# Performance work log

Hardware: AMD Instinct MI355X
Metric: run time of the kernel (lower is better)

Reference implementation:

```python
import jax, jax.numpy as jnp
import numpy as np

P = 2  # lrtd_pad (p_l == p_r == p_t == p_d)
B, C, H, W = 4, 64, 128, 128


def setup_inputs() -> dict:
    key = jax.random.key(0)
    x = jax.random.normal(key, (B, 6, C, H, W), dtype=jnp.float32)
    return {"x": x}


def _cube_pad(x):
    # faces: [B,C,H,W] each; order matches torch module unpacking
    fb, fd, ff, fl, fr, ft = (x[:, i] for i in range(6))
    flip_h = lambda a: a[:, :, ::-1, :]   # flip along dim 2 (rows)
    flip_w = lambda a: a[:, :, :, ::-1]   # flip along dim 3 (cols)
    T = lambda a: jnp.swapaxes(a, 2, 3)   # permute(0,1,3,2)

    # top strips for faces 0..5 -> [B,6,C,P,W]
    top = jnp.stack([
        flip_h(ft[:, :, :P, :]),           # back
        ff[:, :, -P:, :],                  # down
        ft[:, :, -P:, :],                  # front
        T(ft[:, :, :, :P]),                # left
        flip_h(T(ft[:, :, :, -P:])),       # right
        flip_h(fb[:, :, :P, :]),           # top
    ], axis=1)

    # bottom strips -> [B,6,C,P,W]
    bot = jnp.stack([
        flip_h(fd[:, :, -P:, :]),
        flip_h(fb[:, :, -P:, :]),
        fd[:, :, :P, :],
        flip_h(T(fd[:, :, :, :P])),
        T(fd[:, :, :, -P:]),
        ff[:, :, :P, :],
    ], axis=1)

    # left strips -> [B,6,C,H,P]
    lft = jnp.stack([
        fr[:, :, :, -P:],
        flip_w(T(fl[:, :, -P:, :])),
        fl[:, :, :, -P:],
        fb[:, :, :, -P:],
        ff[:, :, :, -P:],
        T(fl[:, :, :P, :]),
    ], axis=1)

    # right strips -> [B,6,C,H,P]
    rgt = jnp.stack([
        fl[:, :, :, :P],
        T(fr[:, :, -P:, :]),
        fr[:, :, :, :P],
        ff[:, :, :, :P],
        fb[:, :, :, :P],
        flip_w(T(fr[:, :, :P, :])),
    ], axis=1)

    # corners: equal pads -> repeat the top/bottom strip's edge column along width
    p_tl = jnp.tile(top[:, :, :, :P, :1], (1, 1, 1, 1, P))
    p_tr = jnp.tile(top[:, :, :, -P:, -1:], (1, 1, 1, 1, P))
    p_dl = jnp.tile(bot[:, :, :, :P, :1], (1, 1, 1, 1, P))
    p_dr = jnp.tile(bot[:, :, :, -P:, -1:], (1, 1, 1, 1, P))

    mid = jnp.concatenate([top, x, bot], axis=3)            # [B,6,C,H+2P,W]
    left = jnp.concatenate([p_tl, lft, p_dl], axis=3)       # [B,6,C,H+2P,P]
    right = jnp.concatenate([p_tr, rgt, p_dr], axis=3)      # [B,6,C,H+2P,P]
    return jnp.concatenate([left, mid, right], axis=4)      # [B,6,C,H+2P,W+2P]


def reference(x):
    return _cube_pad(x)
```

## Files before the change

### kernel.cpp

```cpp
#include <hip/hip_runtime.h>


typedef float f32x4 __attribute__((ext_vector_type(4)));
typedef f32x4 f32x4_a8 __attribute__((aligned(8)));

constexpr int P = 2, B = 4, C = 64, H = 128, W = 128;
constexpr int Ho = H + 2 * P, Wo = W + 2 * P;
constexpr int NV = Wo / 4;
constexpr int PLANES = B * 6 * C;

constexpr int NHALO    = PLANES * 4 * NV;
constexpr int BLK_HALO = NHALO / 256;
constexpr int BANDS    = PLANES * (H / 8);
constexpr int BLOCKS   = BLK_HALO + BANDS;

__device__ __forceinline__ void top_map(int f, int t, int w, int& sf, int& r, int& col) {
    switch (f) {
        case 0:  sf = 5; r = P - 1 - t; col = w;         break;
        case 1:  sf = 2; r = H - P + t; col = w;         break;
        case 2:  sf = 5; r = H - P + t; col = w;         break;
        case 3:  sf = 5; r = w;         col = t;         break;
        case 4:  sf = 5; r = w;         col = W - 1 - t; break;
        default: sf = 0; r = P - 1 - t; col = w;         break;
    }
}
__device__ __forceinline__ void bot_map(int f, int t, int w, int& sf, int& r, int& col) {
    switch (f) {
        case 0:  sf = 1; r = H - 1 - t; col = w;         break;
        case 1:  sf = 0; r = H - 1 - t; col = w;         break;
        case 2:  sf = 1; r = t;         col = w;         break;
        case 3:  sf = 1; r = w;         col = P - 1 - t; break;
        case 4:  sf = 1; r = w;         col = W - P + t; break;
        default: sf = 2; r = t;         col = w;         break;
    }
}
__device__ __forceinline__ void lft_map(int f, int h, int l, int& sf, int& r, int& col) {
    switch (f) {
        case 0:  sf = 4; r = h;         col = W - P + l; break;
        case 1:  sf = 3; r = H - 1 - l; col = h;         break;
        case 2:  sf = 3; r = h;         col = W - P + l; break;
        case 3:  sf = 0; r = h;         col = W - P + l; break;
        case 4:  sf = 2; r = h;         col = W - P + l; break;
        default: sf = 3; r = l;         col = h;         break;
    }
}
__device__ __forceinline__ void rgt_map(int f, int h, int rr, int& sf, int& r, int& col) {
    switch (f) {
        case 0:  sf = 3; r = h;          col = rr;        break;
        case 1:  sf = 4; r = H - P + rr; col = h;         break;
        case 2:  sf = 4; r = h;          col = rr;        break;
        case 3:  sf = 2; r = h;          col = rr;        break;
        case 4:  sf = 0; r = h;          col = rr;        break;
        default: sf = 4; r = P - 1 - rr; col = h;         break;
    }
}

__device__ __forceinline__ void gen_map(int f, int i, int j, int& sf, int& r, int& col) {
    bool in_h = (i >= P) && (i < H + P);
    bool in_w = (j >= P) && (j < W + P);
    if (in_h && in_w) {
        sf = f; r = i - P; col = j - P;
    } else if (!in_h) {
        int w = in_w ? (j - P) : (j < P ? 0 : W - 1);
        if (i < P) top_map(f, i, w, sf, r, col);
        else       bot_map(f, i - H - P, w, sf, r, col);
    } else {
        if (j < P) lft_map(f, i - P, j,         sf, r, col);
        else       rgt_map(f, i - P, j - W - P, sf, r, col);
    }
}

__global__ __launch_bounds__(256) void cubepad_v10_kernel(const float* __restrict__ x,
                                                          float* __restrict__ out) {
    __shared__ float lds[8 * W];
    const int bid = blockIdx.x;
    const int tid = threadIdx.x;

    if (bid >= BLK_HALO) {
        const int band = bid - BLK_HALO;
        const int p    = band >> 4;
        const int r0   = (band & 15) << 3;
        const int f    = (p >> 6) % 6;
        const int bC   = ((p >> 6) / 6) * (6 * C) + (p & 63);
        const float* plane = x + (size_t)p * (H * W);

        {
            const int r = tid >> 5, g = tid & 31;
            const f32x4 v = *(const f32x4*)(plane + ((size_t)(r0 + r) << 7) + (g << 2));
            *(f32x4*)(&lds[tid << 2]) = v;
        }
        __syncthreads();

        const size_t ob = (size_t)p * (Ho * Wo);
        for (int m = tid; m < 8 * NV; m += 256) {
            const unsigned r = (unsigned)m / 33u;
            const int g = m - (int)(r * 33u);
            const int i = r0 + (int)r;
            f32x4 o;
            if (g == 0) {
                int sf, rr, cc;
                lft_map(f, i, 0, sf, rr, cc);
                o[0] = x[((size_t)(bC + sf * C)) * (H * W) + ((size_t)rr << 7) + cc];
                lft_map(f, i, 1, sf, rr, cc);
                o[1] = x[((size_t)(bC + sf * C)) * (H * W) + ((size_t)rr << 7) + cc];
                o[2] = lds[(r << 7) + 0];
                o[3] = lds[(r << 7) + 1];
            } else if (g == NV - 1) {
                o[0] = lds[(r << 7) + 126];
                o[1] = lds[(r << 7) + 127];
                int sf, rr, cc;
                rgt_map(f, i, 0, sf, rr, cc);
                o[2] = x[((size_t)(bC + sf * C)) * (H * W) + ((size_t)rr << 7) + cc];
                rgt_map(f, i, 1, sf, rr, cc);
                o[3] = x[((size_t)(bC + sf * C)) * (H * W) + ((size_t)rr << 7) + cc];
            } else {
                o = *(const f32x4_a8*)(&lds[(r << 7) + (g << 2) - 2]);
            }
            __builtin_nontemporal_store(
                o, (f32x4*)(out + ob + (size_t)(i + P) * Wo + ((size_t)g << 2)));
        }
        return;
    }

    const unsigned h  = (unsigned)bid * 256u + (unsigned)tid;
    const unsigned v  = h % (unsigned)NV;
    const unsigned t2 = h / (unsigned)NV;
    const unsigned t  = t2 & 3u;
    const unsigned p  = t2 >> 2;
    const int i_out = (t < 2u) ? (int)t : (H + P + (int)t - 2);
    const int f  = (int)((p >> 6) % 6u);
    const int bC = (int)(((p >> 6) / 6u) * (6u * C) + (p & 63u));

    f32x4 val;
    #pragma unroll
    for (int e = 0; e < 4; ++e) {
        int sf, r, col;
        gen_map(f, i_out, (int)(4u * v) + e, sf, r, col);
        val[e] = x[((size_t)(bC + sf * C)) * (H * W) + ((size_t)r << 7) + col];
    }
    const size_t o = (size_t)p * (Ho * Wo) + (size_t)i_out * Wo + ((size_t)v << 2);
    __builtin_nontemporal_store(val, (f32x4*)(out + o));
}

extern "C" void kernel_launch(void* const* d_in, const int* in_sizes, int n_in,
                              void* d_out, int out_size, void* d_ws, size_t ws_size,
                              hipStream_t stream) {
    const float* x = (const float*)d_in[0];
    float* out = (float*)d_out;
    cubepad_v10_kernel<<<BLOCKS, 256, 0, stream>>>(x, out);
}
```

Measured before the change: 186.5 us.

## Replace LDS-staged interior band copy with direct per-thread 16-float row segments

The interior path no longer stages 8-row bands through shared memory with a barrier. Each thread now copies a 16-float segment of one row straight from global memory, using unaligned 8-byte-aligned vector loads, and writes it out with nontemporal stores. The first and last thread of each row also gather the left and right halo values. This removes the LDS round trip, the __syncthreads, and the divide-by-33 index math. In exchange the loads are misaligned and each thread issues more work, which may reduce coalescing efficiency.

```diff
diff --git a/kernel.cpp b/kernel.cpp
--- a/kernel.cpp
+++ b/kernel.cpp
@@ -8,11 +8,12 @@
 constexpr int Ho = H + 2 * P, Wo = W + 2 * P;
 constexpr int NV = Wo / 4;
 constexpr int PLANES = B * 6 * C;
+constexpr int ROWS   = PLANES * H;
 
 constexpr int NHALO    = PLANES * 4 * NV;
 constexpr int BLK_HALO = NHALO / 256;
-constexpr int BANDS    = PLANES * (H / 8);
-constexpr int BLOCKS   = BLK_HALO + BANDS;
+constexpr int BLK_INT  = ROWS * 8 / 256;
+constexpr int BLOCKS   = BLK_HALO + BLK_INT;
 
 __device__ __forceinline__ void top_map(int f, int t, int w, int& sf, int& r, int& col) {
     switch (f) {
@@ -54,7 +55,6 @@
         default: sf = 4; r = P - 1 - rr; col = h;         break;
     }
 }
-
 __device__ __forceinline__ void gen_map(int f, int i, int j, int& sf, int& r, int& col) {
     bool in_h = (i >= P) && (i < H + P);
     bool in_w = (j >= P) && (j < W + P);
@@ -70,54 +70,70 @@
     }
 }
 
-__global__ __launch_bounds__(256) void cubepad_v10_kernel(const float* __restrict__ x,
+__global__ __launch_bounds__(256) void cubepad_v11_kernel(const float* __restrict__ x,
                                                           float* __restrict__ out) {
-    __shared__ float lds[8 * W];
     const int bid = blockIdx.x;
     const int tid = threadIdx.x;
 
     if (bid >= BLK_HALO) {
-        const int band = bid - BLK_HALO;
-        const int p    = band >> 4;
-        const int r0   = (band & 15) << 3;
-        const int f    = (p >> 6) % 6;
-        const int bC   = ((p >> 6) / 6) * (6 * C) + (p & 63);
-        const float* plane = x + (size_t)p * (H * W);
+        const unsigned idx = (unsigned)(bid - BLK_HALO) * 256u + (unsigned)tid;
+        const unsigned k   = idx & 7u;
+        const unsigned row = idx >> 3;
+        const unsigned i   = row & 127u;
+        const unsigned p   = row >> 7;
+        const int f  = (int)((p >> 6) % 6u);
+        const int bC = (int)(((p >> 6) / 6u) * (6u * C) + (p & 63u));
 
-        {
-            const int r = tid >> 5, g = tid & 31;
-            const f32x4 v = *(const f32x4*)(plane + ((size_t)(r0 + r) << 7) + (g << 2));
-            *(f32x4*)(&lds[tid << 2]) = v;
-        }
-        __syncthreads();
+        const float* rowp = x + ((size_t)row << 7);
+        float* op = out + (size_t)p * (Ho * Wo) + (size_t)(i + P) * Wo;
 
-        const size_t ob = (size_t)p * (Ho * Wo);
-        for (int m = tid; m < 8 * NV; m += 256) {
-            const unsigned r = (unsigned)m / 33u;
-            const int g = m - (int)(r * 33u);
-            const int i = r0 + (int)r;
-            f32x4 o;
-            if (g == 0) {
-                int sf, rr, cc;
-                lft_map(f, i, 0, sf, rr, cc);
-                o[0] = x[((size_t)(bC + sf * C)) * (H * W) + ((size_t)rr << 7) + cc];
-                lft_map(f, i, 1, sf, rr, cc);
-                o[1] = x[((size_t)(bC + sf * C)) * (H * W) + ((size_t)rr << 7) + cc];
-                o[2] = lds[(r << 7) + 0];
-                o[3] = lds[(r << 7) + 1];
-            } else if (g == NV - 1) {
-                o[0] = lds[(r << 7) + 126];
-                o[1] = lds[(r << 7) + 127];
-                int sf, rr, cc;
-                rgt_map(f, i, 0, sf, rr, cc);
-                o[2] = x[((size_t)(bC + sf * C)) * (H * W) + ((size_t)rr << 7) + cc];
-                rgt_map(f, i, 1, sf, rr, cc);
-                o[3] = x[((size_t)(bC + sf * C)) * (H * W) + ((size_t)rr << 7) + cc];
-            } else {
-                o = *(const f32x4_a8*)(&lds[(r << 7) + (g << 2) - 2]);
-            }
-            __builtin_nontemporal_store(
-                o, (f32x4*)(out + ob + (size_t)(i + P) * Wo + ((size_t)g << 2)));
+        if (k - 1u < 6u) {
+            const float* s = rowp + (k << 4) - 2u;
+            const f32x4 a = *(const f32x4_a8*)(s);
+            const f32x4 b = *(const f32x4_a8*)(s + 4);
+            const f32x4 c = *(const f32x4_a8*)(s + 8);
+            const f32x4 d = *(const f32x4_a8*)(s + 12);
+            float* o = op + (k << 4);
+            __builtin_nontemporal_store(a, (f32x4*)(o));
+            __builtin_nontemporal_store(b, (f32x4*)(o + 4));
+            __builtin_nontemporal_store(c, (f32x4*)(o + 8));
+            __builtin_nontemporal_store(d, (f32x4*)(o + 12));
+        } else if (k == 0u) {
+            const float2 t = *(const float2*)(rowp);
+            const f32x4 a = *(const f32x4_a8*)(rowp + 2);
+            const f32x4 b = *(const f32x4_a8*)(rowp + 6);
+            const f32x4 c = *(const f32x4_a8*)(rowp + 10);
+            int sf, rr, cc;
+            f32x4 e;
+            lft_map(f, (int)i, 0, sf, rr, cc);
+            e[0] = x[((size_t)(bC + sf * C)) * (H * W) + ((size_t)rr << 7) + cc];
+            lft_map(f, (int)i, 1, sf, rr, cc);
+            e[1] = x[((size_t)(bC + sf * C)) * (H * W) + ((size_t)rr << 7) + cc];
+            e[2] = t.x; e[3] = t.y;
+            __builtin_nontemporal_store(e, (f32x4*)(op));
+            __builtin_nontemporal_store(a, (f32x4*)(op + 4));
+            __builtin_nontemporal_store(b, (f32x4*)(op + 8));
+            __builtin_nontemporal_store(c, (f32x4*)(op + 12));
+        } else {
+            const float* s = rowp + 110;
+            const f32x4 a = *(const f32x4_a8*)(s);
+            const f32x4 b = *(const f32x4_a8*)(s + 4);
+            const f32x4 c = *(const f32x4_a8*)(s + 8);
+            const f32x4 d = *(const f32x4_a8*)(s + 12);
+            const float2 t = *(const float2*)(rowp + 126);
+            int sf, rr, cc;
+            f32x4 e;
+            rgt_map(f, (int)i, 0, sf, rr, cc);
+            e[2] = x[((size_t)(bC + sf * C)) * (H * W) + ((size_t)rr << 7) + cc];
+            rgt_map(f, (int)i, 1, sf, rr, cc);
+            e[3] = x[((size_t)(bC + sf * C)) * (H * W) + ((size_t)rr << 7) + cc];
+            e[0] = t.x; e[1] = t.y;
+            float* o = op + 112;
+            __builtin_nontemporal_store(a, (f32x4*)(o));
+            __builtin_nontemporal_store(b, (f32x4*)(o + 4));
+            __builtin_nontemporal_store(c, (f32x4*)(o + 8));
+            __builtin_nontemporal_store(d, (f32x4*)(o + 12));
+            __builtin_nontemporal_store(e, (f32x4*)(o + 16));
         }
         return;
     }
@@ -147,5 +163,5 @@
                               hipStream_t stream) {
     const float* x = (const float*)d_in[0];
     float* out = (float*)d_out;
-    cubepad_v10_kernel<<<BLOCKS, 256, 0, stream>>>(x, out);
+    cubepad_v11_kernel<<<BLOCKS, 256, 0, stream>>>(x, out);
 }
```

Result: slower. 294.0 us (+57.6%).
